# Optimization experiments

Measured on AMD Instinct MI355X. Metric: run time of the kernel, lower is better.

## Reference

```python
import jax, jax.numpy as jnp
import numpy as np

# DeepSeek MLA prefill pipeline (absorbed form), matching the GEMM/bmm/sparse-attention
# Dims: m=512 tokens, hidden=7168, d_kv_c=512, d_q_c=1536, d_r=64, d_q=d_kv=128,
# h=16 local heads, attention dim d = d_kv_c + d_r = 576, s_kv=4096, topk=512.

M, HID = 512, 7168
D_KV_C, D_Q_C, D_R, D_Q, D_KV = 512, 1536, 64, 128, 128
H = 16
S_KV, TOPK = 4096, 512
D_ATT = D_KV_C + D_R  # 576


def setup_inputs() -> dict:
    key = jax.random.key(0)
    ks = jax.random.split(key, 8)
    s = lambda n: 1.0 / np.sqrt(n).astype(np.float32)
    return {
        "x": jax.random.normal(ks[0], (M, HID), jnp.float32),
        "W_cqkv": jax.random.normal(ks[1], (HID, D_KV_C + D_Q_C + D_R), jnp.float32) * s(HID),
        "W_uq": jax.random.normal(ks[2], (D_Q_C, H * (D_Q + D_R)), jnp.float32) * s(D_Q_C),
        "W_qk": jax.random.normal(ks[3], (H, D_Q, D_KV_C), jnp.float32) * s(D_Q),
        "kv_cache": jax.random.normal(ks[4], (S_KV, D_ATT), jnp.float32),
        "W_o1": jax.random.normal(ks[5], (H, D_KV_C, D_KV), jnp.float32) * s(D_KV_C),
        "W_oproj": jax.random.normal(ks[6], (H * D_KV, HID), jnp.float32) * s(H * D_KV),
        "indices": jax.random.randint(ks[7], (M, TOPK), 0, S_KV, jnp.int32),
    }


def reference(x, W_cqkv, W_uq, W_qk, kv_cache, W_o1, W_oproj, indices):
    # 1) QKV compression GEMM: [m, hid] @ [hid, d_kv_c + d_q_c + d_r]
    c = x @ W_cqkv
    kv_c_new = c[:, :D_KV_C]                      # compressed KV (would extend cache)
    q_c = c[:, D_KV_C:D_KV_C + D_Q_C]             # [m, d_q_c]
    # (kv_c_new / k_r_new feed the cache in a real pipeline; attention below reads

    # 2) Q uncompression GEMM: [m, d_q_c] @ [d_q_c, h*(d_q+d_r)]
    q = (q_c @ W_uq).reshape(M, H, D_Q + D_R)
    q_nope, q_pe = q[..., :D_Q], q[..., D_Q:]     # [m,h,128], [m,h,64]

    # 3) Q absorb bmm: per-head [m, d_q] @ [d_q, d_kv_c]
    q_abs = jnp.einsum('mhq,hqc->mhc', q_nope, W_qk)
    q_full = jnp.concatenate([q_abs, q_pe], axis=-1)  # [m, h, 576]

    # 4) Top-k sparse MLA attention (flash_mla_sparse_fwd math):
    #    indices shared across heads (h_kv = 1); gather kv rows per query token.
    kv_g = kv_cache[indices]                      # [m, topk, 576]
    sm_scale = 1.0 / jnp.sqrt(jnp.float32(D_ATT))
    scores = jnp.einsum('mhd,mtd->mht', q_full, kv_g) * sm_scale
    attn = jax.nn.softmax(scores, axis=-1)        # [m, h, topk]
    o = jnp.einsum('mht,mtc->mhc', attn, kv_g[..., :D_KV_C])  # value = first d_kv_c dims

    # 5) O bmm: per-head [m, d_kv_c] @ [d_kv_c, d_kv]
    o2 = jnp.einsum('mhc,hcv->mhv', o, W_o1)      # [m, h, 128]

    # 6) O projection GEMM: [m, h*d_kv] @ [h*d_kv, hid]
    out = o2.reshape(M, H * D_KV) @ W_oproj       # [m, hid]
    return out
```

## Files before the change

kernel.cpp:

```cpp
#include <hip/hip_runtime.h>
#include <hip/hip_bf16.h>

#define M_DIM 512
#define HID 7168
#define D_KV_C 512
#define D_Q_C 1536
#define D_R 64
#define D_Q 128
#define D_KV 128
#define H_DIM 16
#define S_KV 4096
#define TOPK 512
#define D_ATT 576
#define SPLIT 4
#define SROWS 128
#define SM_SCALE (1.0f / 24.0f)

typedef _Float16 half_t;
typedef __attribute__((ext_vector_type(8))) _Float16 f16x8_t;
typedef __attribute__((ext_vector_type(4))) float f32x4_t;
typedef __attribute__((ext_vector_type(2))) unsigned int u32x2_t;

#define MFMA_F16(a, b, c) __builtin_amdgcn_mfma_f32_16x16x32_f16((a), (b), (c), 0, 0, 0)

__device__ __forceinline__ unsigned lds_addr32(const void* p) {
    return (unsigned)(unsigned long long)(const __attribute__((address_space(3))) char*)p;
}

typedef const __attribute__((address_space(1))) unsigned int* gptr_t;
typedef __attribute__((address_space(3))) unsigned int* lptr_t;
__device__ __forceinline__ void gload_lds16(const void* g, void* l) {
    __builtin_amdgcn_global_load_lds((gptr_t)g, (lptr_t)l, 16, 0, 0);
}

__global__ __launch_bounds__(256) void cvt_f16(const float* __restrict__ src,
                                               half_t* __restrict__ dst, int n8)
{
    int i = blockIdx.x * 256 + threadIdx.x;
    if (i >= n8) return;
    const float4* s = (const float4*)src + (size_t)i * 2;
    float4 a = s[0], b = s[1];
    f16x8_t o;
    o[0] = (half_t)a.x; o[1] = (half_t)a.y; o[2] = (half_t)a.z; o[3] = (half_t)a.w;
    o[4] = (half_t)b.x; o[5] = (half_t)b.y; o[6] = (half_t)b.z; o[7] = (half_t)b.w;
    *(f16x8_t*)(dst + (size_t)i * 8) = o;
}

template<int NS>
__global__ __launch_bounds__(256) void cvt_sum(const float* __restrict__ src, long long slice,
                                               half_t* __restrict__ dst, int n8)
{
    int i = blockIdx.x * 256 + threadIdx.x;
    if (i >= n8) return;
    float a[8] = {};
    #pragma unroll
    for (int s = 0; s < NS; s++) {
        const float4* p = (const float4*)(src + (size_t)s * slice) + (size_t)i * 2;
        float4 u = p[0], v = p[1];
        a[0] += u.x; a[1] += u.y; a[2] += u.z; a[3] += u.w;
        a[4] += v.x; a[5] += v.y; a[6] += v.z; a[7] += v.w;
    }
    f16x8_t o;
    #pragma unroll
    for (int j = 0; j < 8; j++) o[j] = (half_t)a[j];
    *(f16x8_t*)(dst + (size_t)i * 8) = o;
}

__global__ __launch_bounds__(256) void cvt_sum_q(const float* __restrict__ src, long long slice,
                                                 half_t* __restrict__ q16, half_t* __restrict__ qf)
{
    int i = blockIdx.x * 256 + threadIdx.x;
    if (i >= M_DIM * 3072 / 8) return;
    float a[8] = {};
    #pragma unroll
    for (int s = 0; s < 2; s++) {
        const float4* p = (const float4*)(src + (size_t)s * slice) + (size_t)i * 2;
        float4 u = p[0], v = p[1];
        a[0] += u.x; a[1] += u.y; a[2] += u.z; a[3] += u.w;
        a[4] += v.x; a[5] += v.y; a[6] += v.z; a[7] += v.w;
    }
    f16x8_t o;
    #pragma unroll
    for (int j = 0; j < 8; j++) o[j] = (half_t)a[j];
    *(f16x8_t*)(q16 + (size_t)i * 8) = o;
    int col = (i * 8) % 3072;
    int c = col % 192;
    if (c >= 128) {
        int row = (i * 8) / 3072, h = col / 192;
        int mh = row * 16 + h;
        f16x8_t os;
        #pragma unroll
        for (int j = 0; j < 8; j++) os[j] = (half_t)(a[j] * SM_SCALE);
        *(f16x8_t*)(qf + (size_t)mh * D_ATT + D_KV_C + (c - 128)) = os;
    }
}

__global__ __launch_bounds__(256) void cvt_t(
    const float* __restrict__ src, int ld_src, long long sS,
    half_t* __restrict__ dst, int ld_dst, long long sD)
{
    src += (size_t)blockIdx.z * sS;
    dst += (size_t)blockIdx.z * sD;
    int k0 = blockIdx.y * 64, n0 = blockIdx.x * 64;
    __shared__ half_t t[64][80];
    int tid = threadIdx.x;
    int kr = tid >> 4, nc = (tid & 15) * 4;
    #pragma unroll
    for (int i = 0; i < 4; i++) {
        float4 v = *(const float4*)&src[(size_t)(k0 + kr + i * 16) * ld_src + n0 + nc];
        t[nc + 0][kr + i * 16] = (half_t)v.x;
        t[nc + 1][kr + i * 16] = (half_t)v.y;
        t[nc + 2][kr + i * 16] = (half_t)v.z;
        t[nc + 3][kr + i * 16] = (half_t)v.w;
    }
    __syncthreads();
    int nr = tid >> 2, kc = (tid & 3) * 16;
    f16x8_t w0 = *(const f16x8_t*)&t[nr][kc];
    f16x8_t w1 = *(const f16x8_t*)&t[nr][kc + 8];
    *(f16x8_t*)&dst[(size_t)(n0 + nr) * ld_dst + k0 + kc] = w0;
    *(f16x8_t*)&dst[(size_t)(n0 + nr) * ld_dst + k0 + kc + 8] = w1;
}

template<bool F16OUT>
__global__ __launch_bounds__(256) void gemm_f16t(
    const half_t* __restrict__ A, int lda, long long sA,
    const half_t* __restrict__ Bt, int ldb, long long sB,
    void* __restrict__ Cv, int ldc, long long sC, int K, float alpha)
{
    A  += (size_t)blockIdx.z * sA;
    Bt += (size_t)blockIdx.z * sB;
    const int bm = blockIdx.y * 64, bn = blockIdx.x * 64;

    __shared__ __align__(16) char lds[2][16384];

    const int tid = threadIdx.x, w = tid >> 6, lane = tid & 63;
    const int l15 = lane & 15, q = lane >> 4;
    const int wr = w >> 1, wc = w & 1;

    const half_t* gA[2];
    const half_t* gB[2];
    #pragma unroll
    for (int p = 0; p < 2; p++) {
        int c = p * 64 + lane;
        int rl = c >> 3;
        int sg = (c & 7) ^ (rl & 7);
        gA[p] = A  + (size_t)(bm + w * 16 + rl) * lda + sg * 8;
        gB[p] = Bt + (size_t)(bn + w * 16 + rl) * ldb + sg * 8;
    }

    f32x4_t acc[2][2];
    #pragma unroll
    for (int i = 0; i < 2; i++)
        #pragma unroll
        for (int j = 0; j < 2; j++) acc[i][j] = (f32x4_t){0.f, 0.f, 0.f, 0.f};

    const int nsteps = K >> 6;

    {
        char* ab = lds[0];
        char* bb = ab + 8192;
        #pragma unroll
        for (int p = 0; p < 2; p++) {
            gload_lds16(gA[p], ab + w * 2048 + p * 1024);
            gload_lds16(gB[p], bb + w * 2048 + p * 1024);
        }
    }
    __syncthreads();

    int cur = 0;
    for (int s = 0; s < nsteps; s++) {
        if (s + 1 < nsteps) {
            int k0 = (s + 1) << 6;
            char* ab = lds[cur ^ 1];
            char* bb = ab + 8192;
            #pragma unroll
            for (int p = 0; p < 2; p++) {
                gload_lds16(gA[p] + k0, ab + w * 2048 + p * 1024);
                gload_lds16(gB[p] + k0, bb + w * 2048 + p * 1024);
            }
        }
        {
            const char* ab = lds[cur];
            const char* bb = ab + 8192;
            #pragma unroll
            for (int kk = 0; kk < 2; kk++) {
                f16x8_t av[2], bv[2];
                #pragma unroll
                for (int i = 0; i < 2; i++) {
                    int ra = wr * 32 + i * 16 + l15;
                    av[i] = *(const f16x8_t*)(ab + ra * 128 + (((kk * 4 + q) ^ (ra & 7)) * 16));
                    int rb = wc * 32 + i * 16 + l15;
                    bv[i] = *(const f16x8_t*)(bb + rb * 128 + (((kk * 4 + q) ^ (rb & 7)) * 16));
                }
                #pragma unroll
                for (int i = 0; i < 2; i++)
                    #pragma unroll
                    for (int j = 0; j < 2; j++)
                        acc[i][j] = MFMA_F16(av[i], bv[j], acc[i][j]);
            }
        }
        __syncthreads();
        cur ^= 1;
    }

    half_t* Ch = (half_t*)Cv + (F16OUT ? (size_t)blockIdx.z * sC : 0);
    float*  Cf = (float*)Cv  + (F16OUT ? 0 : (size_t)blockIdx.z * sC);
    #pragma unroll
    for (int i = 0; i < 2; i++)
        #pragma unroll
        for (int j = 0; j < 2; j++)
            #pragma unroll
            for (int r = 0; r < 4; r++) {
                size_t row = bm + wr * 32 + i * 16 + q * 4 + r;
                size_t col = bn + wc * 32 + j * 16 + l15;
                float v = acc[i][j][r] * alpha;
                if (F16OUT) Ch[row * ldc + col] = (half_t)v;
                else        Cf[row * ldc + col] = v;
            }
}

__global__ __launch_bounds__(512, 8) void attn_split(
    const half_t* __restrict__ qf,
    const half_t* __restrict__ kvb,
    const int* __restrict__ indices,
    half_t* __restrict__ op,
    float2* __restrict__ ml)
{
    const int m = blockIdx.x, sp = blockIdx.y;
    const int tid = threadIdx.x;
    const int w = tid >> 6, lane = tid & 63;
    const int l15 = lane & 15, q = lane >> 4;

    __shared__ __align__(16) char vbuf[32768];
    __shared__ __align__(16) unsigned short p_s[16 * SROWS];
    __shared__ float red_m[16][8];
    __shared__ float red_s[16][8];

    const int* idxp = indices + (size_t)m * TOPK + sp * SROWS;

    {
        #pragma unroll
        for (int j = 0; j < 4; j++) {
            int R = 4 * w + j;
            int grow = idxp[R];
            unsigned swz = (((unsigned)(R & 7)) << 4) ^ (((unsigned)((R >> 3) & 3)) << 5);
            const char* src = (const char*)(kvb + (size_t)grow * D_ATT) + (((unsigned)(16 * lane)) ^ swz);
            gload_lds16(src, vbuf + R * 1024);
        }
    }

    const int rows0 = idxp[w * 16 + l15];

    f32x4_t acc0 = (f32x4_t){0.f, 0.f, 0.f, 0.f};

    const half_t* qp  = qf  + ((size_t)m * 16 + l15) * D_ATT + q * 8;
    const half_t* kp0 = kvb + (size_t)rows0 * D_ATT + q * 8;

    #pragma unroll
    for (int kk = 0; kk < 18; kk++) {
        f16x8_t ah = *(const f16x8_t*)(qp  + kk * 32);
        f16x8_t b0 = *(const f16x8_t*)(kp0 + kk * 32);
        acc0 = MFMA_F16(ah, b0, acc0);
    }

    float gm[4], e0[4];
    #pragma unroll
    for (int r = 0; r < 4; r++) {
        float mx = acc0[r];
        #pragma unroll
        for (int off = 8; off; off >>= 1) mx = fmaxf(mx, __shfl_xor(mx, off, 16));
        if (l15 == 0) red_m[q * 4 + r][w] = mx;
    }
    __syncthreads();
    #pragma unroll
    for (int r = 0; r < 4; r++) {
        int h = q * 4 + r;
        float mx = red_m[h][0];
        #pragma unroll
        for (int ww = 1; ww < 8; ww++) mx = fmaxf(mx, red_m[h][ww]);
        gm[r] = mx;
        e0[r] = __expf(acc0[r] - mx);
        float s = e0[r];
        #pragma unroll
        for (int off = 8; off; off >>= 1) s += __shfl_xor(s, off, 16);
        if (l15 == 0) red_s[h][w] = s;
    }
    __syncthreads();
    if (w == 0 && l15 == 0) {
        #pragma unroll
        for (int r = 0; r < 4; r++) {
            int h = q * 4 + r;
            float s = 0.f;
            #pragma unroll
            for (int ww = 0; ww < 8; ww++) s += red_s[h][ww];
            ml[(size_t)sp * (M_DIM * H_DIM) + m * 16 + h] = make_float2(gm[r], s);
        }
    }
    #pragma unroll
    for (int r = 0; r < 4; r++) {
        int h = q * 4 + r;
        int t0 = w * 16 + l15;
        union { half_t hh; unsigned short u; } c0;
        c0.hh = (half_t)e0[r];
        p_s[h * SROWS + ((((unsigned)(t0 * 2)) ^ (((unsigned)(h & 7)) << 4)) >> 1)] = c0.u;
    }
    __syncthreads();

    f32x4_t oacc[4];
    #pragma unroll
    for (int i = 0; i < 4; i++) oacc[i] = (f32x4_t){0.f, 0.f, 0.f, 0.f};

    const int row1 = q * 8 + (l15 >> 2);
    const int row2 = row1 + 4;
    const unsigned sw1 = (((unsigned)(row1 & 7)) << 4) ^ (((unsigned)((row1 >> 3) & 3)) << 5);
    const unsigned sw2 = (((unsigned)(row2 & 7)) << 4) ^ (((unsigned)((row2 >> 3) & 3)) << 5);
    const unsigned cbyte = (unsigned)((l15 & 3) * 8);
    const unsigned vb = lds_addr32(vbuf);

    #pragma unroll 1
    for (int ct = 0; ct < SPLIT; ct++) {
        f16x8_t pa;
        {
            unsigned pbyte = ((unsigned)(ct * 64 + q * 16)) ^ (((unsigned)(l15 & 7)) << 4);
            pa = *(const f16x8_t*)((const char*)p_s + l15 * (SROWS * 2) + pbyte);
        }

        u32x2_t blo[4], bhi[4];
        #pragma unroll
        for (int i = 0; i < 4; i++) {
            unsigned c2 = ((unsigned)((w * 4 + i) * 32)) + cbyte;
            unsigned a1 = vb + (unsigned)row1 * 1024u + (c2 ^ sw1);
            unsigned a2 = vb + (unsigned)row2 * 1024u + (c2 ^ sw2);
            asm volatile("ds_read_b64_tr_b16 %0, %1 offset:0" : "=v"(blo[i]) : "v"(a1) : "memory");
            asm volatile("ds_read_b64_tr_b16 %0, %1 offset:0" : "=v"(bhi[i]) : "v"(a2) : "memory");
        }
        asm volatile("s_waitcnt lgkmcnt(0)" ::: "memory");
        __builtin_amdgcn_sched_barrier(0);

        __builtin_amdgcn_s_setprio(1);
        #pragma unroll
        for (int i = 0; i < 4; i++) {
            union { f16x8_t s; struct { u32x2_t lo, hi; } u; } f;
            f.u.lo = blo[i]; f.u.hi = bhi[i];
            oacc[i] = MFMA_F16(pa, f.s, oacc[i]);
        }
        __builtin_amdgcn_s_setprio(0);

        __syncthreads();

        if (ct < SPLIT - 1) {
            #pragma unroll
            for (int j = 0; j < 4; j++) {
                int R = 4 * w + j;
                int grow = idxp[(ct + 1) * 32 + R];
                unsigned swz = (((unsigned)(R & 7)) << 4) ^ (((unsigned)((R >> 3) & 3)) << 5);
                const char* src = (const char*)(kvb + (size_t)grow * D_ATT) + (((unsigned)(16 * lane)) ^ swz);
                gload_lds16(src, vbuf + R * 1024);
            }
            __syncthreads();
        }
    }

    half_t* ob = op + ((size_t)sp * M_DIM + m) * (H_DIM * D_KV_C);
    #pragma unroll
    for (int i = 0; i < 4; i++) {
        int c = (w * 4 + i) * 16 + l15;
        #pragma unroll
        for (int r = 0; r < 4; r++)
            ob[(size_t)(q * 4 + r) * D_KV_C + c] = (half_t)oacc[i][r];
    }
}

__global__ __launch_bounds__(256) void attn_merge(
    half_t* __restrict__ op,
    const float2* __restrict__ ml)
{
    int idx = blockIdx.x * 256 + threadIdx.x;
    if (idx >= M_DIM * H_DIM * D_KV_C / 8) return;
    int mh = idx >> 6;
    int c8 = (idx & 63) * 8;
    float2 a[SPLIT];
    #pragma unroll
    for (int s = 0; s < SPLIT; s++) a[s] = ml[s * (M_DIM * H_DIM) + mh];
    float Mx = a[0].x;
    #pragma unroll
    for (int s = 1; s < SPLIT; s++) Mx = fmaxf(Mx, a[s].x);
    float ws[SPLIT], denom = 0.f;
    #pragma unroll
    for (int s = 0; s < SPLIT; s++) { ws[s] = __expf(a[s].x - Mx); denom += ws[s] * a[s].y; }
    float inv = 1.0f / denom;
    float acc[8] = {};
    #pragma unroll
    for (int s = 0; s < SPLIT; s++) {
        f16x8_t v = *(const f16x8_t*)(op + ((size_t)s * (M_DIM * H_DIM) + mh) * D_KV_C + c8);
        float wn = ws[s] * inv;
        #pragma unroll
        for (int j = 0; j < 8; j++) acc[j] += wn * (float)v[j];
    }
    f16x8_t o8;
    #pragma unroll
    for (int j = 0; j < 8; j++) o8[j] = (half_t)acc[j];
    *(f16x8_t*)(op + (size_t)mh * D_KV_C + c8) = o8;
}

extern "C" void kernel_launch(void* const* d_in, const int* in_sizes, int n_in,
                              void* d_out, int out_size, void* d_ws, size_t ws_size,
                              hipStream_t stream)
{
    const float* x        = (const float*)d_in[0];
    const float* W_cqkv   = (const float*)d_in[1];
    const float* W_uq     = (const float*)d_in[2];
    const float* W_qk     = (const float*)d_in[3];
    const float* kv_cache = (const float*)d_in[4];
    const float* W_o1     = (const float*)d_in[5];
    const float* W_oproj  = (const float*)d_in[6];
    const int*   indices  = (const int*)d_in[7];
    float* out = (float*)d_out;

    half_t* wsh = (half_t*)d_ws;
    half_t* Wcqkv_t = wsh;
    half_t* qc16    = wsh;
    half_t* o_part  = wsh;
    half_t* o16     = wsh;
    half_t* q32h    = wsh + 786432;
    half_t* q16     = wsh + 7077888;
    half_t* x16     = wsh + 11010048;
    half_t* Wuq_t   = wsh + 14680064;
    half_t* o2_16   = wsh + 16777216;
    half_t* Wqk_t   = wsh + 19398656;
    half_t* ml_h    = wsh + 19398656;
    half_t* Wo1_t   = wsh + 20447232;
    half_t* Wop_t   = wsh + 21495808;
    half_t* kv16    = wsh + 36175872;
    half_t* qc32h   = wsh + 38535168;
    half_t* qf16    = wsh + 38535168;
    float*  qc32 = (float*)qc32h;
    float*  q32  = (float*)q32h;
    float2* ml   = (float2*)ml_h;

    cvt_f16<<<(M_DIM * HID / 8 + 255) / 256, 256, 0, stream>>>(x, x16, M_DIM * HID / 8);
    cvt_f16<<<(S_KV * D_ATT / 8 + 255) / 256, 256, 0, stream>>>(kv_cache, kv16, S_KV * D_ATT / 8);
    cvt_t<<<dim3(D_Q_C / 64, HID / 64, 1), 256, 0, stream>>>(
        W_cqkv + D_KV_C, D_KV_C + D_Q_C + D_R, 0, Wcqkv_t, HID, 0);
    cvt_t<<<dim3(3072 / 64, D_Q_C / 64, 1), 256, 0, stream>>>(
        W_uq, 3072, 0, Wuq_t, D_Q_C, 0);
    cvt_t<<<dim3(D_KV_C / 64, D_Q / 64, H_DIM), 256, 0, stream>>>(
        W_qk, D_KV_C, D_Q * D_KV_C, Wqk_t, D_Q, D_Q * D_KV_C);
    cvt_t<<<dim3(D_KV / 64, D_KV_C / 64, H_DIM), 256, 0, stream>>>(
        W_o1, D_KV, D_KV_C * D_KV, Wo1_t, D_KV_C, D_KV_C * D_KV);
    cvt_t<<<dim3(HID / 64, 2048 / 64, 1), 256, 0, stream>>>(
        W_oproj, HID, 0, Wop_t, 2048, 0);

    gemm_f16t<false><<<dim3(D_Q_C / 64, M_DIM / 64, 4), 256, 0, stream>>>(
        x16, HID, 1792, Wcqkv_t, HID, 1792, qc32, D_Q_C, (long long)M_DIM * D_Q_C, 1792, 1.0f);
    cvt_sum<4><<<(M_DIM * D_Q_C / 8 + 255) / 256, 256, 0, stream>>>(
        qc32, (long long)M_DIM * D_Q_C, qc16, M_DIM * D_Q_C / 8);

    gemm_f16t<false><<<dim3(3072 / 64, M_DIM / 64, 2), 256, 0, stream>>>(
        qc16, D_Q_C, 768, Wuq_t, D_Q_C, 768, q32, 3072, (long long)M_DIM * 3072, 768, 1.0f);
    cvt_sum_q<<<(M_DIM * 3072 / 8 + 255) / 256, 256, 0, stream>>>(
        q32, (long long)M_DIM * 3072, q16, qf16);

    gemm_f16t<true><<<dim3(D_KV_C / 64, M_DIM / 64, H_DIM), 256, 0, stream>>>(
        q16, 3072, D_Q + D_R, Wqk_t, D_Q, (long long)D_Q * D_KV_C,
        qf16, H_DIM * D_ATT, D_ATT, D_Q, SM_SCALE);

    attn_split<<<dim3(M_DIM, SPLIT), 512, 0, stream>>>(qf16, kv16, indices, o_part, ml);
    attn_merge<<<(M_DIM * H_DIM * D_KV_C / 8 + 255) / 256, 256, 0, stream>>>(o_part, ml);

    gemm_f16t<true><<<dim3(D_KV / 64, M_DIM / 64, H_DIM), 256, 0, stream>>>(
        o16, H_DIM * D_KV_C, D_KV_C, Wo1_t, D_KV_C, (long long)D_KV_C * D_KV,
        o2_16, H_DIM * D_KV, D_KV, D_KV_C, 1.0f);

    gemm_f16t<false><<<dim3(HID / 64, M_DIM / 64, 1), 256, 0, stream>>>(
        o2_16, H_DIM * D_KV, 0, Wop_t, 2048, 0, out, HID, 0, 2048, 1.0f);
}
```

Measured before the change: 232.7 us.

## Reuse QK-phase register loads of KV rows as V tiles in double-buffered LDS

The attention split kernel now keeps the first 512 dims of each gathered KV row, already loaded into registers for the score MFMA, and writes them into LDS instead of issuing a second global gather for the value tiles. LDS is double-buffered: each pair of waves writes its 32 rows into the next buffer while the current chunk is consumed, which removes the extra barrier per chunk. The cost is 16 extra f16x8 vector registers per thread, double the LDS footprint, and occupancy hint lowered from 8 to 4 blocks.

```diff
diff --git a/kernel.cpp b/kernel.cpp
--- a/kernel.cpp
+++ b/kernel.cpp
@@ -219,7 +219,7 @@
             }
 }
 
-__global__ __launch_bounds__(512, 8) void attn_split(
+__global__ __launch_bounds__(512, 4) void attn_split(
     const half_t* __restrict__ qf,
     const half_t* __restrict__ kvb,
     const int* __restrict__ indices,
@@ -231,24 +231,13 @@
     const int w = tid >> 6, lane = tid & 63;
     const int l15 = lane & 15, q = lane >> 4;
 
-    __shared__ __align__(16) char vbuf[32768];
+    __shared__ __align__(16) char vbuf[2][32768];
     __shared__ __align__(16) unsigned short p_s[16 * SROWS];
     __shared__ float red_m[16][8];
     __shared__ float red_s[16][8];
 
     const int* idxp = indices + (size_t)m * TOPK + sp * SROWS;
 
-    {
-        #pragma unroll
-        for (int j = 0; j < 4; j++) {
-            int R = 4 * w + j;
-            int grow = idxp[R];
-            unsigned swz = (((unsigned)(R & 7)) << 4) ^ (((unsigned)((R >> 3) & 3)) << 5);
-            const char* src = (const char*)(kvb + (size_t)grow * D_ATT) + (((unsigned)(16 * lane)) ^ swz);
-            gload_lds16(src, vbuf + R * 1024);
-        }
-    }
-
     const int rows0 = idxp[w * 16 + l15];
 
     f32x4_t acc0 = (f32x4_t){0.f, 0.f, 0.f, 0.f};
@@ -256,9 +245,16 @@
     const half_t* qp  = qf  + ((size_t)m * 16 + l15) * D_ATT + q * 8;
     const half_t* kp0 = kvb + (size_t)rows0 * D_ATT + q * 8;
 
-    #pragma unroll
-    for (int kk = 0; kk < 18; kk++) {
-        f16x8_t ah = *(const f16x8_t*)(qp  + kk * 32);
+    f16x8_t v[16];
+    #pragma unroll
+    for (int kk = 0; kk < 16; kk++) {
+        f16x8_t ah = *(const f16x8_t*)(qp + kk * 32);
+        v[kk] = *(const f16x8_t*)(kp0 + kk * 32);
+        acc0 = MFMA_F16(ah, v[kk], acc0);
+    }
+    #pragma unroll
+    for (int kk = 16; kk < 18; kk++) {
+        f16x8_t ah = *(const f16x8_t*)(qp + kk * 32);
         f16x8_t b0 = *(const f16x8_t*)(kp0 + kk * 32);
         acc0 = MFMA_F16(ah, b0, acc0);
     }
@@ -304,6 +300,18 @@
         c0.hh = (half_t)e0[r];
         p_s[h * SROWS + ((((unsigned)(t0 * 2)) ^ (((unsigned)(h & 7)) << 4)) >> 1)] = c0.u;
     }
+
+    const int Rw = (w & 1) * 16 + l15;
+    const unsigned swzw = (((unsigned)(Rw & 7)) << 4) ^ (((unsigned)((Rw >> 3) & 3)) << 5);
+
+    if ((w >> 1) == 0) {
+        char* buf = vbuf[0];
+        #pragma unroll
+        for (int kk = 0; kk < 16; kk++) {
+            unsigned c = ((unsigned)(q * 16 + kk * 64)) ^ swzw;
+            *(f16x8_t*)(buf + Rw * 1024 + c) = v[kk];
+        }
+    }
     __syncthreads();
 
     f32x4_t oacc[4];
@@ -315,10 +323,20 @@
     const unsigned sw1 = (((unsigned)(row1 & 7)) << 4) ^ (((unsigned)((row1 >> 3) & 3)) << 5);
     const unsigned sw2 = (((unsigned)(row2 & 7)) << 4) ^ (((unsigned)((row2 >> 3) & 3)) << 5);
     const unsigned cbyte = (unsigned)((l15 & 3) * 8);
-    const unsigned vb = lds_addr32(vbuf);
 
     #pragma unroll 1
     for (int ct = 0; ct < SPLIT; ct++) {
+        if (ct < SPLIT - 1 && (w >> 1) == ct + 1) {
+            char* buf = vbuf[(ct + 1) & 1];
+            #pragma unroll
+            for (int kk = 0; kk < 16; kk++) {
+                unsigned c = ((unsigned)(q * 16 + kk * 64)) ^ swzw;
+                *(f16x8_t*)(buf + Rw * 1024 + c) = v[kk];
+            }
+        }
+
+        const unsigned vb = lds_addr32(vbuf[ct & 1]);
+
         f16x8_t pa;
         {
             unsigned pbyte = ((unsigned)(ct * 64 + q * 16)) ^ (((unsigned)(l15 & 7)) << 4);
@@ -347,18 +365,6 @@
         __builtin_amdgcn_s_setprio(0);
 
         __syncthreads();
-
-        if (ct < SPLIT - 1) {
-            #pragma unroll
-            for (int j = 0; j < 4; j++) {
-                int R = 4 * w + j;
-                int grow = idxp[(ct + 1) * 32 + R];
-                unsigned swz = (((unsigned)(R & 7)) << 4) ^ (((unsigned)((R >> 3) & 3)) << 5);
-                const char* src = (const char*)(kvb + (size_t)grow * D_ATT) + (((unsigned)(16 * lane)) ^ swz);
-                gload_lds16(src, vbuf + R * 1024);
-            }
-            __syncthreads();
-        }
     }
 
     half_t* ob = op + ((size_t)sp * M_DIM + m) * (H_DIM * D_KV_C);
```

After: 237.4 us. Within noise of the previous version (+2.0%).

## Stage full KV rows in LDS once and use 1024-thread attention blocks

Applied to the files above, without the earlier changes.

The attention split kernel now loads each gathered 576-wide KV row for its 128-row chunk into shared memory once. The QK score MFMAs read K from LDS instead of re-reading global memory, and the PV stage reuses the same buffer, so the per-chunk reload and barrier loop is gone. Blocks grow to 16 waves: the QK reduction is split across two wave halves and combined through LDS, and PV columns are split two per wave. This cuts redundant global gathers and barriers, but raises LDS use to about 150KB per block, which limits occupancy to one block per CU. The q16 workspace offset also moves and cvt_sum_q gains a template parameter.

```diff
diff --git a/kernel.cpp b/kernel.cpp
--- a/kernel.cpp
+++ b/kernel.cpp
@@ -66,6 +66,7 @@
     *(f16x8_t*)(dst + (size_t)i * 8) = o;
 }
 
+template<int NS>
 __global__ __launch_bounds__(256) void cvt_sum_q(const float* __restrict__ src, long long slice,
                                                  half_t* __restrict__ q16, half_t* __restrict__ qf)
 {
@@ -73,7 +74,7 @@
     if (i >= M_DIM * 3072 / 8) return;
     float a[8] = {};
     #pragma unroll
-    for (int s = 0; s < 2; s++) {
+    for (int s = 0; s < NS; s++) {
         const float4* p = (const float4*)(src + (size_t)s * slice) + (size_t)i * 2;
         float4 u = p[0], v = p[1];
         a[0] += u.x; a[1] += u.y; a[2] += u.z; a[3] += u.w;
@@ -219,7 +220,7 @@
             }
 }
 
-__global__ __launch_bounds__(512, 8) void attn_split(
+__global__ __launch_bounds__(1024, 4) void attn_split(
     const half_t* __restrict__ qf,
     const half_t* __restrict__ kvb,
     const int* __restrict__ indices,
@@ -231,59 +232,74 @@
     const int w = tid >> 6, lane = tid & 63;
     const int l15 = lane & 15, q = lane >> 4;
 
-    __shared__ __align__(16) char vbuf[32768];
+    __shared__ __align__(16) char kbuf[SROWS * 1152];
     __shared__ __align__(16) unsigned short p_s[16 * SROWS];
+    __shared__ __align__(16) float pred[8][64][4];
     __shared__ float red_m[16][8];
     __shared__ float red_s[16][8];
 
     const int* idxp = indices + (size_t)m * TOPK + sp * SROWS;
 
-    {
-        #pragma unroll
-        for (int j = 0; j < 4; j++) {
-            int R = 4 * w + j;
-            int grow = idxp[R];
-            unsigned swz = (((unsigned)(R & 7)) << 4) ^ (((unsigned)((R >> 3) & 3)) << 5);
-            const char* src = (const char*)(kvb + (size_t)grow * D_ATT) + (((unsigned)(16 * lane)) ^ swz);
-            gload_lds16(src, vbuf + R * 1024);
-        }
-    }
-
-    const int rows0 = idxp[w * 16 + l15];
+    #pragma unroll
+    for (int i = 0; i < 9; i++) {
+        int cbase = i * 1024 + w * 64;
+        int c = cbase + lane;
+        int R = c / 72;
+        int xo = (c - R * 72) * 16;
+        unsigned swz = (((unsigned)(R & 7)) << 4) ^ (((unsigned)((R >> 3) & 3)) << 5);
+        const char* src = (const char*)(kvb + (size_t)idxp[R] * D_ATT) + (((unsigned)xo) ^ swz);
+        gload_lds16(src, kbuf + (size_t)cbase * 16);
+    }
+
+    const int tg = w & 7, half = w >> 3;
+    const int R0 = tg * 16 + l15;
+    const unsigned swzR = (((unsigned)(R0 & 7)) << 4) ^ (((unsigned)((R0 >> 3) & 3)) << 5);
+    const half_t* qp = qf + ((size_t)m * 16 + l15) * D_ATT + q * 8;
 
     f32x4_t acc0 = (f32x4_t){0.f, 0.f, 0.f, 0.f};
 
-    const half_t* qp  = qf  + ((size_t)m * 16 + l15) * D_ATT + q * 8;
-    const half_t* kp0 = kvb + (size_t)rows0 * D_ATT + q * 8;
-
-    #pragma unroll
-    for (int kk = 0; kk < 18; kk++) {
-        f16x8_t ah = *(const f16x8_t*)(qp  + kk * 32);
-        f16x8_t b0 = *(const f16x8_t*)(kp0 + kk * 32);
+    __syncthreads();
+
+    #pragma unroll
+    for (int k2 = 0; k2 < 9; k2++) {
+        int kk = half * 9 + k2;
+        f16x8_t ah = *(const f16x8_t*)(qp + kk * 32);
+        f16x8_t b0 = *(const f16x8_t*)(kbuf + R0 * 1152 + (((unsigned)(kk * 64 + q * 16)) ^ swzR));
         acc0 = MFMA_F16(ah, b0, acc0);
     }
 
+    if (half) *(f32x4_t*)&pred[tg][lane][0] = acc0;
+    __syncthreads();
+    if (!half) {
+        f32x4_t o = *(const f32x4_t*)&pred[tg][lane][0];
+        acc0[0] += o[0]; acc0[1] += o[1]; acc0[2] += o[2]; acc0[3] += o[3];
+    }
+
     float gm[4], e0[4];
-    #pragma unroll
-    for (int r = 0; r < 4; r++) {
-        float mx = acc0[r];
-        #pragma unroll
-        for (int off = 8; off; off >>= 1) mx = fmaxf(mx, __shfl_xor(mx, off, 16));
-        if (l15 == 0) red_m[q * 4 + r][w] = mx;
-    }
-    __syncthreads();
-    #pragma unroll
-    for (int r = 0; r < 4; r++) {
-        int h = q * 4 + r;
-        float mx = red_m[h][0];
-        #pragma unroll
-        for (int ww = 1; ww < 8; ww++) mx = fmaxf(mx, red_m[h][ww]);
-        gm[r] = mx;
-        e0[r] = __expf(acc0[r] - mx);
-        float s = e0[r];
-        #pragma unroll
-        for (int off = 8; off; off >>= 1) s += __shfl_xor(s, off, 16);
-        if (l15 == 0) red_s[h][w] = s;
+    if (!half) {
+        #pragma unroll
+        for (int r = 0; r < 4; r++) {
+            float mx = acc0[r];
+            #pragma unroll
+            for (int off = 8; off; off >>= 1) mx = fmaxf(mx, __shfl_xor(mx, off, 16));
+            if (l15 == 0) red_m[q * 4 + r][tg] = mx;
+        }
+    }
+    __syncthreads();
+    if (!half) {
+        #pragma unroll
+        for (int r = 0; r < 4; r++) {
+            int h = q * 4 + r;
+            float mx = red_m[h][0];
+            #pragma unroll
+            for (int ww = 1; ww < 8; ww++) mx = fmaxf(mx, red_m[h][ww]);
+            gm[r] = mx;
+            e0[r] = __expf(acc0[r] - mx);
+            float s = e0[r];
+            #pragma unroll
+            for (int off = 8; off; off >>= 1) s += __shfl_xor(s, off, 16);
+            if (l15 == 0) red_s[h][tg] = s;
+        }
     }
     __syncthreads();
     if (w == 0 && l15 == 0) {
@@ -296,41 +312,46 @@
             ml[(size_t)sp * (M_DIM * H_DIM) + m * 16 + h] = make_float2(gm[r], s);
         }
     }
-    #pragma unroll
-    for (int r = 0; r < 4; r++) {
-        int h = q * 4 + r;
-        int t0 = w * 16 + l15;
-        union { half_t hh; unsigned short u; } c0;
-        c0.hh = (half_t)e0[r];
-        p_s[h * SROWS + ((((unsigned)(t0 * 2)) ^ (((unsigned)(h & 7)) << 4)) >> 1)] = c0.u;
-    }
-    __syncthreads();
-
-    f32x4_t oacc[4];
-    #pragma unroll
-    for (int i = 0; i < 4; i++) oacc[i] = (f32x4_t){0.f, 0.f, 0.f, 0.f};
-
-    const int row1 = q * 8 + (l15 >> 2);
-    const int row2 = row1 + 4;
-    const unsigned sw1 = (((unsigned)(row1 & 7)) << 4) ^ (((unsigned)((row1 >> 3) & 3)) << 5);
-    const unsigned sw2 = (((unsigned)(row2 & 7)) << 4) ^ (((unsigned)((row2 >> 3) & 3)) << 5);
+    if (!half) {
+        #pragma unroll
+        for (int r = 0; r < 4; r++) {
+            int h = q * 4 + r;
+            int t0 = tg * 16 + l15;
+            union { half_t hh; unsigned short u; } c0;
+            c0.hh = (half_t)e0[r];
+            p_s[h * SROWS + ((((unsigned)(t0 * 2)) ^ (((unsigned)(h & 7)) << 4)) >> 1)] = c0.u;
+        }
+    }
+    __syncthreads();
+
+    f32x4_t oacc[2];
+    oacc[0] = (f32x4_t){0.f, 0.f, 0.f, 0.f};
+    oacc[1] = (f32x4_t){0.f, 0.f, 0.f, 0.f};
+
+    const unsigned kb = lds_addr32(kbuf);
+    const int r1 = q * 8 + (l15 >> 2);
+    const int r2 = r1 + 4;
     const unsigned cbyte = (unsigned)((l15 & 3) * 8);
-    const unsigned vb = lds_addr32(vbuf);
-
-    #pragma unroll 1
-    for (int ct = 0; ct < SPLIT; ct++) {
+
+    #pragma unroll
+    for (int ct = 0; ct < 4; ct++) {
         f16x8_t pa;
         {
             unsigned pbyte = ((unsigned)(ct * 64 + q * 16)) ^ (((unsigned)(l15 & 7)) << 4);
             pa = *(const f16x8_t*)((const char*)p_s + l15 * (SROWS * 2) + pbyte);
         }
 
-        u32x2_t blo[4], bhi[4];
-        #pragma unroll
-        for (int i = 0; i < 4; i++) {
-            unsigned c2 = ((unsigned)((w * 4 + i) * 32)) + cbyte;
-            unsigned a1 = vb + (unsigned)row1 * 1024u + (c2 ^ sw1);
-            unsigned a2 = vb + (unsigned)row2 * 1024u + (c2 ^ sw2);
+        int Rg1 = ct * 32 + r1;
+        int Rg2 = ct * 32 + r2;
+        unsigned s1 = (((unsigned)(Rg1 & 7)) << 4) ^ (((unsigned)((Rg1 >> 3) & 3)) << 5);
+        unsigned s2 = (((unsigned)(Rg2 & 7)) << 4) ^ (((unsigned)((Rg2 >> 3) & 3)) << 5);
+
+        u32x2_t blo[2], bhi[2];
+        #pragma unroll
+        for (int i = 0; i < 2; i++) {
+            unsigned c2 = ((unsigned)((w * 2 + i) * 32)) + cbyte;
+            unsigned a1 = kb + (unsigned)Rg1 * 1152u + (c2 ^ s1);
+            unsigned a2 = kb + (unsigned)Rg2 * 1152u + (c2 ^ s2);
             asm volatile("ds_read_b64_tr_b16 %0, %1 offset:0" : "=v"(blo[i]) : "v"(a1) : "memory");
             asm volatile("ds_read_b64_tr_b16 %0, %1 offset:0" : "=v"(bhi[i]) : "v"(a2) : "memory");
         }
@@ -339,32 +360,18 @@
 
         __builtin_amdgcn_s_setprio(1);
         #pragma unroll
-        for (int i = 0; i < 4; i++) {
+        for (int i = 0; i < 2; i++) {
             union { f16x8_t s; struct { u32x2_t lo, hi; } u; } f;
             f.u.lo = blo[i]; f.u.hi = bhi[i];
             oacc[i] = MFMA_F16(pa, f.s, oacc[i]);
         }
         __builtin_amdgcn_s_setprio(0);
-
-        __syncthreads();
-
-        if (ct < SPLIT - 1) {
-            #pragma unroll
-            for (int j = 0; j < 4; j++) {
-                int R = 4 * w + j;
-                int grow = idxp[(ct + 1) * 32 + R];
-                unsigned swz = (((unsigned)(R & 7)) << 4) ^ (((unsigned)((R >> 3) & 3)) << 5);
-                const char* src = (const char*)(kvb + (size_t)grow * D_ATT) + (((unsigned)(16 * lane)) ^ swz);
-                gload_lds16(src, vbuf + R * 1024);
-            }
-            __syncthreads();
-        }
     }
 
     half_t* ob = op + ((size_t)sp * M_DIM + m) * (H_DIM * D_KV_C);
     #pragma unroll
-    for (int i = 0; i < 4; i++) {
-        int c = (w * 4 + i) * 16 + l15;
+    for (int i = 0; i < 2; i++) {
+        int c = (w * 2 + i) * 16 + l15;
         #pragma unroll
         for (int r = 0; r < 4; r++)
             ob[(size_t)(q * 4 + r) * D_KV_C + c] = (half_t)oacc[i][r];
@@ -423,10 +430,10 @@
     half_t* o_part  = wsh;
     half_t* o16     = wsh;
     half_t* q32h    = wsh + 786432;
-    half_t* q16     = wsh + 7077888;
     half_t* x16     = wsh + 11010048;
+    half_t* q16     = wsh + 13369344;
+    half_t* o2_16   = wsh + 16777216;
     half_t* Wuq_t   = wsh + 14680064;
-    half_t* o2_16   = wsh + 16777216;
     half_t* Wqk_t   = wsh + 19398656;
     half_t* ml_h    = wsh + 19398656;
     half_t* Wo1_t   = wsh + 20447232;
@@ -458,14 +465,14 @@
 
     gemm_f16t<false><<<dim3(3072 / 64, M_DIM / 64, 2), 256, 0, stream>>>(
         qc16, D_Q_C, 768, Wuq_t, D_Q_C, 768, q32, 3072, (long long)M_DIM * 3072, 768, 1.0f);
-    cvt_sum_q<<<(M_DIM * 3072 / 8 + 255) / 256, 256, 0, stream>>>(
+    cvt_sum_q<2><<<(M_DIM * 3072 / 8 + 255) / 256, 256, 0, stream>>>(
         q32, (long long)M_DIM * 3072, q16, qf16);
 
     gemm_f16t<true><<<dim3(D_KV_C / 64, M_DIM / 64, H_DIM), 256, 0, stream>>>(
         q16, 3072, D_Q + D_R, Wqk_t, D_Q, (long long)D_Q * D_KV_C,
         qf16, H_DIM * D_ATT, D_ATT, D_Q, SM_SCALE);
 
-    attn_split<<<dim3(M_DIM, SPLIT), 512, 0, stream>>>(qf16, kv16, indices, o_part, ml);
+    attn_split<<<dim3(M_DIM, SPLIT), 1024, 0, stream>>>(qf16, kv16, indices, o_part, ml);
     attn_merge<<<(M_DIM * H_DIM * D_KV_C / 8 + 255) / 256, 256, 0, stream>>>(o_part, ml);
 
     gemm_f16t<true><<<dim3(D_KV / 64, M_DIM / 64, H_DIM), 256, 0, stream>>>(
```

Measured after the change: 233.7 us. About the same (+0.4%).
